# Performance work log

Hardware: AMD Instinct MI355X
Metric: run time of the kernel (lower is better)

Reference implementation:

```python
import jax, jax.numpy as jnp
import numpy as np

BETA_THRESH = 0.1   # threshold fraction in forward
BETA_IPOT = 0.5     # IPOT entropic beta
ITERATION = 30


def setup_inputs() -> dict:
    key = jax.random.key(0)
    k1, k2 = jax.random.split(key)
    bs, n, m, d = 64, 512, 512, 768
    return {
        "local_features_1": jax.random.normal(k1, (bs, n, d), dtype=jnp.float32),
        "local_features_2": jax.random.normal(k2, (bs, m, d), dtype=jnp.float32),
    }


def _wasserstein_loss(x, y):
    # x: (bs, n, d), y: (bs, m, d)
    # cost_matrix_batch_torch normalizes over the feature dim (dim=1 of bs*d*n layout)
    xn = x / (jnp.linalg.norm(x, axis=2, keepdims=True) + 1e-12)
    yn = y / (jnp.linalg.norm(y, axis=2, keepdims=True) + 1e-12)
    # cost_matrix returns (1 - cos).transpose(2,1); forward transposes back -> (bs, n, m)
    cos_distance = 1.0 - jnp.einsum("bnd,bmd->bnm", xn, yn)
    # global min/max threshold + relu
    min_score = cos_distance.min()
    max_score = cos_distance.max()
    threshold = min_score + BETA_THRESH * (max_score - min_score)
    C = jax.nn.relu(cos_distance - threshold)  # (bs, n, m)
    bs, n, m = C.shape
    A = jnp.exp(-C / BETA_IPOT)
    T0 = jnp.ones((bs, n, m), dtype=C.dtype)
    sigma0 = jnp.full((bs, m, 1), 1.0 / m, dtype=C.dtype)

    def step(carry, _):
        T, sigma = carry
        Q = A * T                                      # (bs, n, m)
        delta = 1.0 / (n * jnp.matmul(Q, sigma))       # (bs, n, 1)
        a = jnp.matmul(jnp.swapaxes(Q, 1, 2), delta)   # (bs, m, 1)
        sigma = 1.0 / (m * a)                          # (bs, m, 1)
        T = delta * Q * jnp.swapaxes(sigma, 1, 2)      # (bs, n, m)
        return (T, sigma), None

    (T, _), _ = jax.lax.scan(step, (T0, sigma0), None, length=ITERATION)
    # batch_trace(C^T @ T) == sum_ij C_ij * T_ij per batch element
    distance = jnp.einsum("bnm,bnm->b", C, T)
    # IPOT_distance returns -distance; loss is its mean
    return (-distance).mean()


def reference(local_features_1, local_features_2):
    return _wasserstein_loss(local_features_1, local_features_2)
```

## Files before the change

kernel.cpp:

```cpp
#include <hip/hip_runtime.h>
#include <hip/hip_fp16.h>

#define NN 512
#define DD 768

typedef _Float16 half8 __attribute__((ext_vector_type(8)));
typedef _Float16 half4 __attribute__((ext_vector_type(4)));
typedef _Float16 half2v __attribute__((ext_vector_type(2)));
typedef float f32x4 __attribute__((ext_vector_type(4)));

__device__ __forceinline__ int f2ord(float f) {
  int i = __float_as_int(f);
  return i < 0 ? (i ^ 0x7fffffff) : i;
}
__device__ __forceinline__ float ord2f(int i) {
  return __int_as_float(i < 0 ? (i ^ 0x7fffffff) : i);
}

__global__ void k_init(int* meta, int* cnt) {
  int t = threadIdx.x;
  if (t == 0) {
    meta[0] = 0x7fffffff;
    meta[1] = 0x80000000;
  }
  if (t < 64) cnt[t * 16] = 0;
}

__global__ __launch_bounds__(256) void k_norm(const float* __restrict__ f1,
                                              const float* __restrict__ f2,
                                              __half* __restrict__ xn,
                                              __half* __restrict__ yn) {
  int row = blockIdx.x * 4 + (threadIdx.x >> 6);
  int lane = threadIdx.x & 63;
  int r = row & 32767;
  const float* src = (row < 32768 ? f1 : f2) + (size_t)r * DD;
  __half* dst = (row < 32768 ? xn : yn) + (size_t)r * DD;
  f32x4 v0 = *(const f32x4*)(src + lane * 4);
  f32x4 v1 = *(const f32x4*)(src + lane * 4 + 256);
  f32x4 v2 = *(const f32x4*)(src + lane * 4 + 512);
  float s = v0[0]*v0[0] + v0[1]*v0[1] + v0[2]*v0[2] + v0[3]*v0[3]
          + v1[0]*v1[0] + v1[1]*v1[1] + v1[2]*v1[2] + v1[3]*v1[3]
          + v2[0]*v2[0] + v2[1]*v2[1] + v2[2]*v2[2] + v2[3]*v2[3];
  #pragma unroll
  for (int m = 1; m < 64; m <<= 1) s += __shfl_xor(s, m, 64);
  float f = 1.0f / (sqrtf(s) + 1e-12f);
  union U { __half2 h2[2]; uint2 u; };
  U u0, u1, u2;
  u0.h2[0] = __floats2half2_rn(v0[0]*f, v0[1]*f); u0.h2[1] = __floats2half2_rn(v0[2]*f, v0[3]*f);
  u1.h2[0] = __floats2half2_rn(v1[0]*f, v1[1]*f); u1.h2[1] = __floats2half2_rn(v1[2]*f, v1[3]*f);
  u2.h2[0] = __floats2half2_rn(v2[0]*f, v2[1]*f); u2.h2[1] = __floats2half2_rn(v2[2]*f, v2[3]*f);
  *(uint2*)(dst + lane * 4)       = u0.u;
  *(uint2*)(dst + lane * 4 + 256) = u1.u;
  *(uint2*)(dst + lane * 4 + 512) = u2.u;
}

__global__ void k_gemm(const __half* __restrict__ xn, const __half* __restrict__ yn,
                       float* __restrict__ cosm, int* __restrict__ meta) {
  __shared__ __align__(16) __half As[4096];
  __shared__ __align__(16) __half Bs[4096];
  __shared__ float rmin[4], rmax[4];
  const int b  = blockIdx.y;
  const int ti = blockIdx.x >> 2;
  const int tj = blockIdx.x & 3;
  const int tid = threadIdx.x;
  const int wv = tid >> 6, lane = tid & 63;
  const int wr = (wv >> 1) * 64, wc = (wv & 1) * 64;
  const __half* Ab = xn + ((size_t)b * NN + (size_t)ti * 128) * DD;
  const __half* Bb = yn + ((size_t)b * NN + (size_t)tj * 128) * DD;
  const int srow = tid >> 2;
  const int scol = (tid & 3) * 8;
  const __half* ga0 = Ab + (size_t)srow * DD + scol;
  const __half* ga1 = ga0 + (size_t)64 * DD;
  const __half* gb0 = Bb + (size_t)srow * DD + scol;
  const __half* gb1 = gb0 + (size_t)64 * DD;
  __half* la0 = As + tid * 8;
  __half* la1 = As + 2048 + tid * 8;
  __half* lb0 = Bs + tid * 8;
  __half* lb1 = Bs + 2048 + tid * 8;
  f32x4 acc[4][4] = {};
  const int fr = lane & 15;
  const int kb = (lane >> 4) * 8;
  typedef _Float16 mhalf8 __attribute__((ext_vector_type(8)));
  uint4 va0 = *(const uint4*)ga0;
  uint4 va1 = *(const uint4*)ga1;
  uint4 vb0 = *(const uint4*)gb0;
  uint4 vb1 = *(const uint4*)gb1;
  for (int kk = 0; kk < DD; kk += 32) {
    __syncthreads();
    *(uint4*)la0 = va0; *(uint4*)la1 = va1;
    *(uint4*)lb0 = vb0; *(uint4*)lb1 = vb1;
    __syncthreads();
    if (kk + 32 < DD) {
      va0 = *(const uint4*)(ga0 + kk + 32);
      va1 = *(const uint4*)(ga1 + kk + 32);
      vb0 = *(const uint4*)(gb0 + kk + 32);
      vb1 = *(const uint4*)(gb1 + kk + 32);
    }
    mhalf8 af[4], bf[4];
    #pragma unroll
    for (int g = 0; g < 4; ++g) {
      af[g] = *(const mhalf8*)(As + (wr + g * 16 + fr) * 32 + kb);
      bf[g] = *(const mhalf8*)(Bs + (wc + g * 16 + fr) * 32 + kb);
    }
    #pragma unroll
    for (int g = 0; g < 4; ++g) {
      #pragma unroll
      for (int h = 0; h < 4; ++h) {
        acc[g][h] = __builtin_amdgcn_mfma_f32_16x16x32_f16(af[g], bf[h], acc[g][h], 0, 0, 0);
      }
    }
  }
  float vmin = 1e30f, vmax = -1e30f;
  float* cb = cosm + (size_t)b * NN * NN;
  #pragma unroll
  for (int g = 0; g < 4; ++g) {
    #pragma unroll
    for (int h = 0; h < 4; ++h) {
      #pragma unroll
      for (int r2 = 0; r2 < 4; ++r2) {
        int row = ti * 128 + wr + g * 16 + (lane >> 4) * 4 + r2;
        int col = tj * 128 + wc + h * 16 + fr;
        float val = 1.0f - acc[g][h][r2];
        cb[(size_t)row * NN + col] = val;
        vmin = fminf(vmin, val); vmax = fmaxf(vmax, val);
      }
    }
  }
  #pragma unroll
  for (int m = 1; m < 64; m <<= 1) {
    vmin = fminf(vmin, __shfl_xor(vmin, m, 64));
    vmax = fmaxf(vmax, __shfl_xor(vmax, m, 64));
  }
  if (lane == 0) { rmin[wv] = vmin; rmax[wv] = vmax; }
  __syncthreads();
  if (tid == 0) {
    float bm = fminf(fminf(rmin[0], rmin[1]), fminf(rmin[2], rmin[3]));
    float bx = fmaxf(fmaxf(rmax[0], rmax[1]), fmaxf(rmax[2], rmax[3]));
    atomicMin(meta + 0, f2ord(bm));
    atomicMax(meta + 1, f2ord(bx));
  }
}

#define FOR16(X) X(0) X(1) X(2) X(3) X(4) X(5) X(6) X(7) X(8) X(9) X(10) X(11) X(12) X(13) X(14) X(15)

__global__ __launch_bounds__(512, 2) void k_ipot(const float* __restrict__ cosm,
                                                 const int* __restrict__ meta,
                                                 int* __restrict__ cnt,
                                                 float* __restrict__ gpart,
                                                 float* __restrict__ gdist) {
  __shared__ float xs[128];
  __shared__ float ys[NN];
  __shared__ __align__(16) _Float16 zs[NN];
  __shared__ __align__(16) _Float16 csh[8][520];
  __shared__ float wred[8];
  const int blk = blockIdx.x;
  const int b = blk & 63, qq = blk >> 6;
  const int tid = threadIdx.x;
  const int w = tid >> 6, lane = tid & 63;
  const int r0 = w * 16;
  const int c0 = lane * 8;
  const float* cb = cosm + (size_t)b * NN * NN + (size_t)(qq * 128) * NN;
  const float gmn = ord2f(meta[0]);
  const float gmx = ord2f(meta[1]);
  const float thr = gmn + 0.1f * (gmx - gmn);

#define DECLAM(r) half8 A##r, M##r;
  FOR16(DECLAM)

#define INITAM(r) { \
    const float* rp = cb + (size_t)(r0 + r) * NN + c0; \
    f32x4 v0 = *(const f32x4*)rp; \
    f32x4 v1 = *(const f32x4*)(rp + 4); \
    A##r.s0 = (_Float16)__expf(-2.0f * fmaxf(v0[0] - thr, 0.0f)); \
    A##r.s1 = (_Float16)__expf(-2.0f * fmaxf(v0[1] - thr, 0.0f)); \
    A##r.s2 = (_Float16)__expf(-2.0f * fmaxf(v0[2] - thr, 0.0f)); \
    A##r.s3 = (_Float16)__expf(-2.0f * fmaxf(v0[3] - thr, 0.0f)); \
    A##r.s4 = (_Float16)__expf(-2.0f * fmaxf(v1[0] - thr, 0.0f)); \
    A##r.s5 = (_Float16)__expf(-2.0f * fmaxf(v1[1] - thr, 0.0f)); \
    A##r.s6 = (_Float16)__expf(-2.0f * fmaxf(v1[2] - thr, 0.0f)); \
    A##r.s7 = (_Float16)__expf(-2.0f * fmaxf(v1[3] - thr, 0.0f)); \
    M##r = A##r; }
  FOR16(INITAM)

  if (tid < 256) *(half2v*)(zs + 2 * tid) = (half2v){(_Float16)1.0f, (_Float16)1.0f};
  ys[tid] = 1.0f;
  __syncthreads();

  int* mycnt = cnt + b * 16;

  #pragma unroll 1
  for (int t = 1; t <= 30; ++t) {
    half8 zv = *(const half8*)(zs + c0);
    float rp16[16];
#define ROWP(r) { \
      half8 p = M##r * zv; \
      half4 q = p.lo + p.hi; \
      half2v q2 = q.lo + q.hi; \
      rp16[r] = (float)q2.x + (float)q2.y; }
    FOR16(ROWP)
    float c8[8];
    #pragma unroll
    for (int i = 0; i < 8; ++i) {
      float keep = (lane & 1) ? rp16[2*i+1] : rp16[2*i];
      float send = (lane & 1) ? rp16[2*i]   : rp16[2*i+1];
      c8[i] = keep + __shfl_xor(send, 1, 64);
    }
    float c4[4];
    #pragma unroll
    for (int i = 0; i < 4; ++i) {
      float keep = (lane & 2) ? c8[2*i+1] : c8[2*i];
      float send = (lane & 2) ? c8[2*i]   : c8[2*i+1];
      c4[i] = keep + __shfl_xor(send, 2, 64);
    }
    float d2[2];
    #pragma unroll
    for (int i = 0; i < 2; ++i) {
      float keep = (lane & 4) ? c4[2*i+1] : c4[2*i];
      float send = (lane & 4) ? c4[2*i]   : c4[2*i+1];
      d2[i] = keep + __shfl_xor(send, 4, 64);
    }
    float c1;
    {
      float keep = (lane & 8) ? d2[1] : d2[0];
      float send = (lane & 8) ? d2[0] : d2[1];
      c1 = keep + __shfl_xor(send, 8, 64);
    }
    c1 += __shfl_xor(c1, 16, 64);
    c1 += __shfl_xor(c1, 32, 64);
    if (lane < 16) xs[r0 + lane] = 1.0f / c1;
    __syncthreads();
    half8 cac = (half8)(_Float16)0.0f;
#define COLP(r) { _Float16 xh = (_Float16)xs[r0 + r]; cac += M##r * xh; }
    FOR16(COLP)
    *(half8*)(&csh[w][c0]) = cac;
#define UPDM(r) M##r *= A##r;
    if (t < 30) { FOR16(UPDM) }
    __syncthreads();
    float* gp = gpart + ((size_t)((t & 1) * 256 + blk) * 512);
    if (tid < 256) {
      float a0 = 0.0f, a1 = 0.0f;
      #pragma unroll
      for (int g = 0; g < 8; ++g) {
        half2v pv = *(const half2v*)(&csh[g][2 * tid]);
        a0 += (float)pv.x; a1 += (float)pv.y;
      }
      __hip_atomic_store(gp + tid * 2,     a0, __ATOMIC_RELAXED, __HIP_MEMORY_SCOPE_AGENT);
      __hip_atomic_store(gp + tid * 2 + 1, a1, __ATOMIC_RELAXED, __HIP_MEMORY_SCOPE_AGENT);
    }
    __syncthreads();
    if (tid == 0) {
      __hip_atomic_fetch_add(mycnt, 1, __ATOMIC_RELAXED, __HIP_MEMORY_SCOPE_AGENT);
      while (__hip_atomic_load(mycnt, __ATOMIC_RELAXED, __HIP_MEMORY_SCOPE_AGENT) < 4 * t)
        __builtin_amdgcn_s_sleep(1);
    }
    __syncthreads();
    if (tid < 256) {
      float a0 = 0.0f, a1 = 0.0f;
      #pragma unroll
      for (int q2 = 0; q2 < 4; ++q2) {
        const float* gpb = gpart + ((size_t)((t & 1) * 256 + b + 64 * q2) * 512);
        a0 += __hip_atomic_load(gpb + tid * 2,     __ATOMIC_RELAXED, __HIP_MEMORY_SCOPE_AGENT);
        a1 += __hip_atomic_load(gpb + tid * 2 + 1, __ATOMIC_RELAXED, __HIP_MEMORY_SCOPE_AGENT);
      }
      float yo0 = ys[2 * tid], yo1 = ys[2 * tid + 1];
      float y0 = 1.0f / a0;
      float y1 = 1.0f / a1;
      *(half2v*)(zs + 2 * tid) = (half2v){(_Float16)(y0 * y0 / yo0), (_Float16)(y1 * y1 / yo1)};
      ys[2 * tid] = y0; ys[2 * tid + 1] = y1;
    }
    __syncthreads();
  }

  float contrib = 0.0f;
#define FINP(r) { \
    const float* rp = cb + (size_t)(r0 + r) * NN + c0; \
    f32x4 v0 = *(const f32x4*)rp; \
    f32x4 v1 = *(const f32x4*)(rp + 4); \
    float rowacc = 0.0f; \
    rowacc += fmaxf(v0[0] - thr, 0.0f) * (float)M##r.s0 * ys[c0 + 0]; \
    rowacc += fmaxf(v0[1] - thr, 0.0f) * (float)M##r.s1 * ys[c0 + 1]; \
    rowacc += fmaxf(v0[2] - thr, 0.0f) * (float)M##r.s2 * ys[c0 + 2]; \
    rowacc += fmaxf(v0[3] - thr, 0.0f) * (float)M##r.s3 * ys[c0 + 3]; \
    rowacc += fmaxf(v1[0] - thr, 0.0f) * (float)M##r.s4 * ys[c0 + 4]; \
    rowacc += fmaxf(v1[1] - thr, 0.0f) * (float)M##r.s5 * ys[c0 + 5]; \
    rowacc += fmaxf(v1[2] - thr, 0.0f) * (float)M##r.s6 * ys[c0 + 6]; \
    rowacc += fmaxf(v1[3] - thr, 0.0f) * (float)M##r.s7 * ys[c0 + 7]; \
    contrib += rowacc * xs[r0 + r]; }
  FOR16(FINP)
  #pragma unroll
  for (int m = 1; m < 64; m <<= 1) contrib += __shfl_xor(contrib, m, 64);
  if (lane == 0) wred[w] = contrib;
  __syncthreads();
  if (tid == 0) {
    float s2 = 0.0f;
    #pragma unroll
    for (int g = 0; g < 8; ++g) s2 += wred[g];
    gdist[blk] = s2;
  }
}

__global__ void k_final(const float* __restrict__ gdist, float* __restrict__ out) {
  int b = threadIdx.x & 63;
  float v = gdist[b] + gdist[b + 64] + gdist[b + 128] + gdist[b + 192];
  #pragma unroll
  for (int m = 1; m < 64; m <<= 1) v += __shfl_xor(v, m, 64);
  if (threadIdx.x == 0) out[0] = -v * (1.0f / (64.0f * 512.0f));
}

extern "C" void kernel_launch(void* const* d_in, const int* in_sizes, int n_in,
                              void* d_out, int out_size, void* d_ws, size_t ws_size,
                              hipStream_t stream) {
  const float* f1 = (const float*)d_in[0];
  const float* f2 = (const float*)d_in[1];
  char* ws = (char*)d_ws;
  __half* xn  = (__half*)(ws + 0);
  __half* yn  = (__half*)(ws + 50331648);
  float* gpart = (float*)(ws + 50331648);
  float* cosm = (float*)(ws + 100663296);
  int*   meta = (int*)(ws + 167772160);
  int*   cnt  = (int*)(ws + 167772160 + 256);
  float* gdist = (float*)(ws + 167772160 + 256 + 4096);

  k_init<<<1, 64, 0, stream>>>(meta, cnt);
  k_norm<<<16384, 256, 0, stream>>>(f1, f2, xn, yn);
  k_gemm<<<dim3(16, 64), 256, 0, stream>>>(xn, yn, cosm, meta);
  k_ipot<<<256, 512, 0, stream>>>(cosm, meta, cnt, gpart, gdist);
  k_final<<<1, 64, 0, stream>>>(gdist, (float*)d_out);
}
```

Before: 237.3 us.

## Use direct global-to-LDS double buffering in GEMM and flag-tagged IPOT exchange

The GEMM now loads tiles straight into LDS with global_load_lds into a double buffer, so there is one barrier per k-step instead of two and no register staging. The IPOT cross-block column-sum exchange drops the counter-plus-barrier handshake. Each partial sum is written with its sign bit set as a ready flag into a per-iteration slot, and each thread polls the four partner slots directly. This needs a memset of the per-iteration exchange buffer before the kernel. One intra-iteration __syncthreads after the xs write is also removed.

```diff
diff --git a/kernel.cpp b/kernel.cpp
--- a/kernel.cpp
+++ b/kernel.cpp
@@ -17,13 +17,16 @@
   return __int_as_float(i < 0 ? (i ^ 0x7fffffff) : i);
 }
 
-__global__ void k_init(int* meta, int* cnt) {
-  int t = threadIdx.x;
-  if (t == 0) {
+__device__ __forceinline__ void glds16(const void* g, void* l) {
+  __builtin_amdgcn_global_load_lds((const __attribute__((address_space(1))) void*)g,
+                                   (__attribute__((address_space(3))) void*)l, 16, 0, 0);
+}
+
+__global__ void k_init(int* meta) {
+  if (threadIdx.x == 0) {
     meta[0] = 0x7fffffff;
     meta[1] = 0x80000000;
   }
-  if (t < 64) cnt[t * 16] = 0;
 }
 
 __global__ __launch_bounds__(256) void k_norm(const float* __restrict__ f1,
@@ -54,10 +57,12 @@
   *(uint2*)(dst + lane * 4 + 512) = u2.u;
 }
 
-__global__ void k_gemm(const __half* __restrict__ xn, const __half* __restrict__ yn,
-                       float* __restrict__ cosm, int* __restrict__ meta) {
-  __shared__ __align__(16) __half As[4096];
-  __shared__ __align__(16) __half Bs[4096];
+__global__ __launch_bounds__(256) void k_gemm(const __half* __restrict__ xn,
+                                              const __half* __restrict__ yn,
+                                              float* __restrict__ cosm,
+                                              int* __restrict__ meta) {
+  __shared__ __align__(16) __half As[2][4096];
+  __shared__ __align__(16) __half Bs[2][4096];
   __shared__ float rmin[4], rmax[4];
   const int b  = blockIdx.y;
   const int ti = blockIdx.x >> 2;
@@ -73,42 +78,35 @@
   const __half* ga1 = ga0 + (size_t)64 * DD;
   const __half* gb0 = Bb + (size_t)srow * DD + scol;
   const __half* gb1 = gb0 + (size_t)64 * DD;
-  __half* la0 = As + tid * 8;
-  __half* la1 = As + 2048 + tid * 8;
-  __half* lb0 = Bs + tid * 8;
-  __half* lb1 = Bs + 2048 + tid * 8;
   f32x4 acc[4][4] = {};
   const int fr = lane & 15;
   const int kb = (lane >> 4) * 8;
-  typedef _Float16 mhalf8 __attribute__((ext_vector_type(8)));
-  uint4 va0 = *(const uint4*)ga0;
-  uint4 va1 = *(const uint4*)ga1;
-  uint4 vb0 = *(const uint4*)gb0;
-  uint4 vb1 = *(const uint4*)gb1;
+
+#define STAGE(bf, kk) { \
+    glds16(ga0 + (kk), &As[bf][wv * 512]); \
+    glds16(ga1 + (kk), &As[bf][2048 + wv * 512]); \
+    glds16(gb0 + (kk), &Bs[bf][wv * 512]); \
+    glds16(gb1 + (kk), &Bs[bf][2048 + wv * 512]); }
+
+  int buf = 0;
+  STAGE(0, 0)
   for (int kk = 0; kk < DD; kk += 32) {
     __syncthreads();
-    *(uint4*)la0 = va0; *(uint4*)la1 = va1;
-    *(uint4*)lb0 = vb0; *(uint4*)lb1 = vb1;
-    __syncthreads();
-    if (kk + 32 < DD) {
-      va0 = *(const uint4*)(ga0 + kk + 32);
-      va1 = *(const uint4*)(ga1 + kk + 32);
-      vb0 = *(const uint4*)(gb0 + kk + 32);
-      vb1 = *(const uint4*)(gb1 + kk + 32);
-    }
-    mhalf8 af[4], bf[4];
+    if (kk + 32 < DD) STAGE(buf ^ 1, kk + 32)
+    half8 af[4], bf4[4];
     #pragma unroll
     for (int g = 0; g < 4; ++g) {
-      af[g] = *(const mhalf8*)(As + (wr + g * 16 + fr) * 32 + kb);
-      bf[g] = *(const mhalf8*)(Bs + (wc + g * 16 + fr) * 32 + kb);
+      af[g]  = *(const half8*)(&As[buf][(wr + g * 16 + fr) * 32 + kb]);
+      bf4[g] = *(const half8*)(&Bs[buf][(wc + g * 16 + fr) * 32 + kb]);
     }
     #pragma unroll
     for (int g = 0; g < 4; ++g) {
       #pragma unroll
       for (int h = 0; h < 4; ++h) {
-        acc[g][h] = __builtin_amdgcn_mfma_f32_16x16x32_f16(af[g], bf[h], acc[g][h], 0, 0, 0);
+        acc[g][h] = __builtin_amdgcn_mfma_f32_16x16x32_f16(af[g], bf4[h], acc[g][h], 0, 0, 0);
       }
     }
+    buf ^= 1;
   }
   float vmin = 1e30f, vmax = -1e30f;
   float* cb = cosm + (size_t)b * NN * NN;
@@ -143,10 +141,12 @@
 
 #define FOR16(X) X(0) X(1) X(2) X(3) X(4) X(5) X(6) X(7) X(8) X(9) X(10) X(11) X(12) X(13) X(14) X(15)
 
+#define AGLD(p) __hip_atomic_load((p), __ATOMIC_RELAXED, __HIP_MEMORY_SCOPE_AGENT)
+#define AGST(p, v) __hip_atomic_store((p), (v), __ATOMIC_RELAXED, __HIP_MEMORY_SCOPE_AGENT)
+
 __global__ __launch_bounds__(512, 2) void k_ipot(const float* __restrict__ cosm,
                                                  const int* __restrict__ meta,
-                                                 int* __restrict__ cnt,
-                                                 float* __restrict__ gpart,
+                                                 unsigned* __restrict__ gx,
                                                  float* __restrict__ gdist) {
   __shared__ float xs[128];
   __shared__ float ys[NN];
@@ -186,8 +186,6 @@
   ys[tid] = 1.0f;
   __syncthreads();
 
-  int* mycnt = cnt + b * 16;
-
   #pragma unroll 1
   for (int t = 1; t <= 30; ++t) {
     half8 zv = *(const half8*)(zs + c0);
@@ -228,7 +226,6 @@
     c1 += __shfl_xor(c1, 16, 64);
     c1 += __shfl_xor(c1, 32, 64);
     if (lane < 16) xs[r0 + lane] = 1.0f / c1;
-    __syncthreads();
     half8 cac = (half8)(_Float16)0.0f;
 #define COLP(r) { _Float16 xh = (_Float16)xs[r0 + r]; cac += M##r * xh; }
     FOR16(COLP)
@@ -236,7 +233,6 @@
 #define UPDM(r) M##r *= A##r;
     if (t < 30) { FOR16(UPDM) }
     __syncthreads();
-    float* gp = gpart + ((size_t)((t & 1) * 256 + blk) * 512);
     if (tid < 256) {
       float a0 = 0.0f, a1 = 0.0f;
       #pragma unroll
@@ -244,27 +240,25 @@
         half2v pv = *(const half2v*)(&csh[g][2 * tid]);
         a0 += (float)pv.x; a1 += (float)pv.y;
       }
-      __hip_atomic_store(gp + tid * 2,     a0, __ATOMIC_RELAXED, __HIP_MEMORY_SCOPE_AGENT);
-      __hip_atomic_store(gp + tid * 2 + 1, a1, __ATOMIC_RELAXED, __HIP_MEMORY_SCOPE_AGENT);
-    }
-    __syncthreads();
-    if (tid == 0) {
-      __hip_atomic_fetch_add(mycnt, 1, __ATOMIC_RELAXED, __HIP_MEMORY_SCOPE_AGENT);
-      while (__hip_atomic_load(mycnt, __ATOMIC_RELAXED, __HIP_MEMORY_SCOPE_AGENT) < 4 * t)
+      unsigned* base = gx + ((size_t)((t - 1) * 64 + b) * 4) * 512 + 2 * tid;
+      AGST(base + qq * 512,     __float_as_uint(a0) | 0x80000000u);
+      AGST(base + qq * 512 + 1, __float_as_uint(a1) | 0x80000000u);
+      unsigned u00, u01, u10, u11, u20, u21, u30, u31;
+      for (;;) {
+        u00 = AGLD(base);        u01 = AGLD(base + 1);
+        u10 = AGLD(base + 512);  u11 = AGLD(base + 513);
+        u20 = AGLD(base + 1024); u21 = AGLD(base + 1025);
+        u30 = AGLD(base + 1536); u31 = AGLD(base + 1537);
+        if ((int)(u00 & u01 & u10 & u11 & u20 & u21 & u30 & u31) < 0) break;
         __builtin_amdgcn_s_sleep(1);
-    }
-    __syncthreads();
-    if (tid < 256) {
-      float a0 = 0.0f, a1 = 0.0f;
-      #pragma unroll
-      for (int q2 = 0; q2 < 4; ++q2) {
-        const float* gpb = gpart + ((size_t)((t & 1) * 256 + b + 64 * q2) * 512);
-        a0 += __hip_atomic_load(gpb + tid * 2,     __ATOMIC_RELAXED, __HIP_MEMORY_SCOPE_AGENT);
-        a1 += __hip_atomic_load(gpb + tid * 2 + 1, __ATOMIC_RELAXED, __HIP_MEMORY_SCOPE_AGENT);
       }
+      float s0 = __uint_as_float(u00 & 0x7fffffffu) + __uint_as_float(u10 & 0x7fffffffu)
+               + __uint_as_float(u20 & 0x7fffffffu) + __uint_as_float(u30 & 0x7fffffffu);
+      float s1 = __uint_as_float(u01 & 0x7fffffffu) + __uint_as_float(u11 & 0x7fffffffu)
+               + __uint_as_float(u21 & 0x7fffffffu) + __uint_as_float(u31 & 0x7fffffffu);
       float yo0 = ys[2 * tid], yo1 = ys[2 * tid + 1];
-      float y0 = 1.0f / a0;
-      float y1 = 1.0f / a1;
+      float y0 = 1.0f / s0;
+      float y1 = 1.0f / s1;
       *(half2v*)(zs + 2 * tid) = (half2v){(_Float16)(y0 * y0 / yo0), (_Float16)(y1 * y1 / yo1)};
       ys[2 * tid] = y0; ys[2 * tid + 1] = y1;
     }
@@ -315,15 +309,15 @@
   char* ws = (char*)d_ws;
   __half* xn  = (__half*)(ws + 0);
   __half* yn  = (__half*)(ws + 50331648);
-  float* gpart = (float*)(ws + 50331648);
+  unsigned* gx = (unsigned*)(ws + 0);
   float* cosm = (float*)(ws + 100663296);
   int*   meta = (int*)(ws + 167772160);
-  int*   cnt  = (int*)(ws + 167772160 + 256);
-  float* gdist = (float*)(ws + 167772160 + 256 + 4096);
-
-  k_init<<<1, 64, 0, stream>>>(meta, cnt);
+  float* gdist = (float*)(ws + 167772160 + 256);
+
+  k_init<<<1, 64, 0, stream>>>(meta);
   k_norm<<<16384, 256, 0, stream>>>(f1, f2, xn, yn);
   k_gemm<<<dim3(16, 64), 256, 0, stream>>>(xn, yn, cosm, meta);
-  k_ipot<<<256, 512, 0, stream>>>(cosm, meta, cnt, gpart, gdist);
+  hipMemsetAsync(gx, 0, (size_t)30 * 64 * 4 * 512 * 4, stream);
+  k_ipot<<<256, 512, 0, stream>>>(cosm, meta, gx, gdist);
   k_final<<<1, 64, 0, stream>>>(gdist, (float*)d_out);
 }
```

Result: slower. 249.0 us (+4.9%).
